# Kernel tuning notes

Hardware: AMD Instinct MI355X
Metric: run time of the kernel (lower is better)

The kernel has to match this reference:

```python
import jax, jax.numpy as jnp
import numpy as np

LN_EPS = 1e-5

def _proj(x, w, b):
    # 1x1 conv: x [B,C,H,W], w [O,C], b [O]
    return jnp.einsum('bchw,oc->bohw', x, w) + b[None, :, None, None]

def _layernorm(x, w, b):
    # normalize over last dim
    mu = jnp.mean(x, axis=-1, keepdims=True)
    var = jnp.mean(jnp.square(x - mu), axis=-1, keepdims=True)
    return (x - mu) * jax.lax.rsqrt(var + LN_EPS) * w + b

def setup_inputs() -> dict:
    key = jax.random.key(0)
    ks = jax.random.split(key, 12)
    C = 256
    d = {
        's3': jax.random.normal(ks[0], (2, C, 64, 64), jnp.float32),
        's4': jax.random.normal(ks[1], (2, C, 32, 64), jnp.float32),
        's5': jax.random.normal(ks[2], (2, C, 16, 64), jnp.float32),
        'qw': jax.random.normal(ks[3], (C, C), jnp.float32) * 0.02,
        'qb': jax.random.normal(ks[4], (C,), jnp.float32) * 0.02,
        'kw': jax.random.normal(ks[5], (C, C), jnp.float32) * 0.02,
        'kb': jax.random.normal(ks[6], (C,), jnp.float32) * 0.02,
        'vw': jax.random.normal(ks[7], (C, C), jnp.float32) * 0.02,
        'vb': jax.random.normal(ks[8], (C,), jnp.float32) * 0.02,
        'ow': jax.random.normal(ks[9], (C, C), jnp.float32) * 0.02,
        'ob': jax.random.normal(ks[10], (C,), jnp.float32) * 0.02,
        'ln_w': jnp.ones((C,), jnp.float32),
        'ln_b': jnp.zeros((C,), jnp.float32),
    }
    return d

def reference(s3, s4, s5, qw, qb, kw, kb, vw, vb, ow, ob, ln_w, ln_b):
    B, C, H, W = s3.shape
    num_heads = 8
    head_dim = C // num_heads
    scale = head_dim ** -0.5

    q = _proj(s3, qw, qb).reshape(B, C, H * W)            # [B,C,Nq]
    k4 = _proj(s4, kw, kb).reshape(B, C, -1)
    k5 = _proj(s5, kw, kb).reshape(B, C, -1)
    v4 = _proj(s4, vw, vb).reshape(B, C, -1)
    v5 = _proj(s5, vw, vb).reshape(B, C, -1)
    k = jnp.concatenate([k4, k5], axis=-1)                # [B,C,Nk]
    v = jnp.concatenate([v4, v5], axis=-1)

    # [B,C,N] -> [B,h,N,d]
    def split_heads(t):
        Bn, Cn, N = t.shape
        return t.transpose(0, 2, 1).reshape(Bn, N, num_heads, head_dim).transpose(0, 2, 1, 3)

    qh, kh, vh = split_heads(q), split_heads(k), split_heads(v)
    attn = jnp.einsum('bhqd,bhkd->bhqk', qh, kh) * scale
    attn = jax.nn.softmax(attn, axis=-1)
    out = jnp.einsum('bhqk,bhkd->bhqd', attn, vh)         # [B,h,Nq,d]
    out = out.transpose(0, 2, 1, 3).reshape(B, H * W, C)  # [B,Nq,C]
    out = out.transpose(0, 2, 1).reshape(B, C, H, W)
    out = _proj(out, ow, ob)
    out = s3 + out
    out_flat = out.reshape(B, C, H * W).transpose(0, 2, 1)  # [B,N,C]
    out_flat = _layernorm(out_flat, ln_w, ln_b)
    return out_flat.transpose(0, 2, 1).reshape(B, C, H, W)
```

## Files before the change

### kernel.cpp

```cpp
#include <hip/hip_runtime.h>

typedef __bf16 bf16;
typedef __bf16 bf16x4 __attribute__((ext_vector_type(4)));
typedef __bf16 bf16x8 __attribute__((ext_vector_type(8)));
typedef _Float16 f16;
typedef _Float16 f16x2 __attribute__((ext_vector_type(2)));
typedef _Float16 f16x8 __attribute__((ext_vector_type(8)));
typedef float f32x4 __attribute__((ext_vector_type(4)));
typedef unsigned int u32x4 __attribute__((ext_vector_type(4)));

#define MFMA16 __builtin_amdgcn_mfma_f32_16x16x32_bf16
#define MFMA16H __builtin_amdgcn_mfma_f32_16x16x32_f16

__device__ __forceinline__ void async16(void* lds, const void* g) {
    __builtin_amdgcn_global_load_lds((const __attribute__((address_space(1))) unsigned int*)g,
                                     (__attribute__((address_space(3))) unsigned int*)lds, 16, 0, 0);
}

__device__ __forceinline__ f16x2 pkrtz(float a, float b) {
    return __builtin_bit_cast(f16x2, __builtin_amdgcn_cvt_pkrtz(a, b));
}

__device__ __forceinline__ float fdot2h(f16x2 a, f16x2 b, float c) {
#if __has_builtin(__builtin_amdgcn_fdot2)
    return __builtin_amdgcn_fdot2(a, b, c, false);
#else
    return c + (float)a[0] * (float)b[0] + (float)a[1] * (float)b[1];
#endif
}

__global__ __launch_bounds__(256) void k_prep(const float* __restrict__ qw, const float* __restrict__ kw,
                                              const float* __restrict__ vw, const float* __restrict__ ow,
                                              bf16* __restrict__ Wb,
                                              const float* __restrict__ s3, const float* __restrict__ s4,
                                              const float* __restrict__ s5,
                                              bf16* __restrict__ s3t, bf16* __restrict__ s45t) {
    __shared__ float T[64][65];
    int bx = blockIdx.x, t = threadIdx.x;
    if (bx < 256) {
        int tt = bx * 256 + t;
        const float* srcs[4] = {qw, kw, vw, ow};
        int which = tt >> 14;
        int idx = (tt & 16383) * 4;
        f32x4 v = *(const f32x4*)(srcs[which] + idx);
        bf16x4 o;
        o[0] = (bf16)v[0]; o[1] = (bf16)v[1]; o[2] = (bf16)v[2]; o[3] = (bf16)v[3];
        *(bf16x4*)(Wb + (size_t)which * 65536 + idx) = o;
        return;
    }
    const float* src; bf16* dst; int N, dstRows, rowOff, x, y, z;
    if (bx < 768)       { int i = bx - 256;  src = s3; dst = s3t;  N = 4096; dstRows = 4096; rowOff = 0;    x = i & 63; y = (i >> 6) & 3; z = i >> 8; }
    else if (bx < 1024) { int i = bx - 768;  src = s4; dst = s45t; N = 2048; dstRows = 3072; rowOff = 0;    x = i & 31; y = (i >> 5) & 3; z = i >> 7; }
    else                { int i = bx - 1024; src = s5; dst = s45t; N = 1024; dstRows = 3072; rowOff = 2048; x = i & 15; y = (i >> 4) & 3; z = i >> 6; }
    int c0 = y * 64, n0 = x * 64, b = z;
    const float* s = src + ((size_t)b * 256 + c0) * N + n0;
#pragma unroll
    for (int i = 0; i < 4; i++) {
        int flat = i * 256 + t;
        int row = flat >> 4;
        int col = (flat & 15) * 4;
        f32x4 v = *(const f32x4*)(s + (size_t)row * N + col);
        T[row][col + 0] = v[0]; T[row][col + 1] = v[1];
        T[row][col + 2] = v[2]; T[row][col + 3] = v[3];
    }
    __syncthreads();
#pragma unroll
    for (int i = 0; i < 4; i++) {
        int flat = i * 256 + t;
        int nrow = flat >> 4;
        int c4 = (flat & 15) * 4;
        bf16x4 o;
        o[0] = (bf16)T[c4 + 0][nrow]; o[1] = (bf16)T[c4 + 1][nrow];
        o[2] = (bf16)T[c4 + 2][nrow]; o[3] = (bf16)T[c4 + 3][nrow];
        *(bf16x4*)(dst + ((size_t)(b * dstRows + rowOff + n0 + nrow)) * 256 + c0 + c4) = o;
    }
}

__global__ __launch_bounds__(256) void k_qkv(const bf16* __restrict__ Wb,
                                             const bf16* __restrict__ s3t, const bf16* __restrict__ s45t,
                                             const float* __restrict__ qb, const float* __restrict__ kb,
                                             const float* __restrict__ vb,
                                             bf16* __restrict__ Qb, bf16* __restrict__ Kb,
                                             f16* __restrict__ Vtb, float qscale) {
    int i = blockIdx.x;
    int mode, n0, m0, b, Nrows;
    const bf16 *A, *Bt; const float* bias; float oscale = 1.0f;
    if (i < 512) {
        mode = 0; A = Wb; Bt = s3t; bias = qb; Nrows = 4096; oscale = qscale;
        n0 = (i & 63) * 64; m0 = ((i >> 6) & 3) * 64; b = i >> 8;
    } else if (i < 896) {
        unsigned j = i - 512;
        mode = 1; A = Wb + 65536; Bt = s45t; bias = kb; Nrows = 3072;
        n0 = (j % 48u) * 64; unsigned rr = j / 48u; m0 = (rr & 3) * 64; b = rr >> 2;
    } else {
        unsigned j = i - 896;
        mode = 2; A = Wb + 131072; Bt = s45t; bias = vb; Nrows = 3072;
        n0 = (j % 48u) * 64; unsigned rr = j / 48u; m0 = (rr & 3) * 64; b = rr >> 2;
    }
    __shared__ bf16 As[64 * 40];
    __shared__ bf16 Bs[64 * 40];
    int t = threadIdx.x;
    int w = t >> 6, lane = t & 63;
    int lrow = lane & 15, lk = lane >> 4;
    f32x4 acc[4] = {};
    int r = t >> 2, cc = (t & 3) * 8;
    for (int kc = 0; kc < 256; kc += 32) {
        u32x4 va = *(const u32x4*)(A + (size_t)(m0 + r) * 256 + kc + cc);
        u32x4 vbv = *(const u32x4*)(Bt + ((size_t)b * Nrows + n0 + r) * 256 + kc + cc);
        *(u32x4*)(As + r * 40 + cc) = va;
        *(u32x4*)(Bs + r * 40 + cc) = vbv;
        __syncthreads();
        bf16x8 af = *(const bf16x8*)(As + (w * 16 + lrow) * 40 + lk * 8);
#pragma unroll
        for (int ct = 0; ct < 4; ct++) {
            bf16x8 bfr = *(const bf16x8*)(Bs + (ct * 16 + lrow) * 40 + lk * 8);
            acc[ct] = MFMA16(af, bfr, acc[ct], 0, 0, 0);
        }
        __syncthreads();
    }
    int o0 = m0 + w * 16 + lk * 4;
    f32x4 b4 = *(const f32x4*)(bias + o0);
    int head = o0 >> 5;
#pragma unroll
    for (int ct = 0; ct < 4; ct++) {
        int n = n0 + ct * 16 + lrow;
        if (mode == 0) {
            int dd = o0 & 31;
            bf16x4 pv;
#pragma unroll
            for (int j = 0; j < 4; j++) pv[j] = (bf16)((acc[ct][j] + b4[j]) * oscale);
            *(bf16x4*)(Qb + ((size_t)(b * 8 + head) * 4096 + n) * 32 + dd) = pv;
        } else if (mode == 1) {
            int dd = o0 & 31;
            int u = n & 31;
            int np = (n & ~31) | (((u >> 2) & 1) << 4) | ((u >> 3) << 2) | (u & 3);
            bf16x4 pv;
#pragma unroll
            for (int j = 0; j < 4; j++) pv[j] = (bf16)(acc[ct][j] + b4[j]);
            *(bf16x4*)(Kb + ((size_t)(b * 8 + head) * 3072 + np) * 32 + dd) = pv;
        } else {
            int g = (n & 63) >> 3;
#pragma unroll
            for (int j = 0; j < 4; j++) {
                int dd = (o0 & 31) + j;
                int col = (n & ~63) + ((g ^ (dd & 7)) << 3) + (n & 7);
                Vtb[((size_t)(b * 8 + head) * 32 + dd) * 3072 + col] = (f16)(acc[ct][j] + b4[j]);
            }
        }
    }
}

__global__ __launch_bounds__(256, 4) void k_attn(const bf16* __restrict__ Q, const bf16* __restrict__ K,
                                                 const f16* __restrict__ Vt,
                                                 f16* __restrict__ Opart, float* __restrict__ Lsum) {
    int bh = blockIdx.y;
    int q0 = blockIdx.x * 256;
    int sp = blockIdx.z;
    int kn0 = sp * 768;
    int t = threadIdx.x, w = t >> 6, lane = t & 63;
    int lrow = lane & 15, lk = lane >> 4;
    __shared__ bf16 Ks[2][64 * 32];
    __shared__ f16 Vs[2][32 * 64];
    __shared__ f16 Tq[4][32 * 66];
    const bf16* kbase = K + (size_t)bh * 3072 * 32;
    const f16* vbase = Vt + (size_t)bh * 32 * 3072;
    const bf16* kg = kbase + (size_t)(kn0 + w * 16 + (lane >> 2)) * 32 + (lane & 3) * 8;
    const f16* vg = vbase + (size_t)(w * 8 + (lane >> 3)) * 3072 + kn0 + (lane & 7) * 8;
    bf16x8 aq[4];
#pragma unroll
    for (int qg = 0; qg < 4; ++qg)
        aq[qg] = *(const bf16x8*)(Q + ((size_t)bh * 4096 + q0 + w * 64 + qg * 16 + lrow) * 32 + lk * 8);
    f32x4 accO[4][2] = {};
    float lsum[4] = {0.f, 0.f, 0.f, 0.f};
    f32x4 zero = {};
    f16x2 one2; one2[0] = (f16)1.f; one2[1] = (f16)1.f;
    int vkey = lrow & 7;
    async16(&Ks[0][w * 512], kg);
    async16(&Vs[0][w * 512], vg);
    __syncthreads();
    for (int c = 0; c < 12; ++c) {
        int buf = c & 1;
        if (c < 11) {
            async16(&Ks[buf ^ 1][w * 512], kg + (size_t)(c + 1) * 64 * 32);
            async16(&Vs[buf ^ 1][w * 512], vg + (c + 1) * 64);
        }
        const bf16* ksb = &Ks[buf][0];
        const f16* vsb = &Vs[buf][0];
#pragma unroll
        for (int p = 0; p < 2; ++p) {
            f32x4 s[2][4];
#pragma unroll
            for (int t2 = 0; t2 < 2; ++t2) {
                bf16x8 kf = *(const bf16x8*)(ksb + (p * 32 + t2 * 16 + lrow) * 32 + lk * 8);
#pragma unroll
                for (int qg = 0; qg < 4; ++qg) s[t2][qg] = MFMA16(kf, aq[qg], zero, 0, 0, 0);
            }
            f16x8 p8[4];
#pragma unroll
            for (int qg = 0; qg < 4; ++qg) {
                f16x2 h0 = pkrtz(__builtin_amdgcn_exp2f(s[0][qg][0]), __builtin_amdgcn_exp2f(s[0][qg][1]));
                f16x2 h1 = pkrtz(__builtin_amdgcn_exp2f(s[0][qg][2]), __builtin_amdgcn_exp2f(s[0][qg][3]));
                f16x2 h2 = pkrtz(__builtin_amdgcn_exp2f(s[1][qg][0]), __builtin_amdgcn_exp2f(s[1][qg][1]));
                f16x2 h3 = pkrtz(__builtin_amdgcn_exp2f(s[1][qg][2]), __builtin_amdgcn_exp2f(s[1][qg][3]));
                f16x8 pk;
                pk[0] = h0[0]; pk[1] = h0[1]; pk[2] = h1[0]; pk[3] = h1[1];
                pk[4] = h2[0]; pk[5] = h2[1]; pk[6] = h3[0]; pk[7] = h3[1];
                p8[qg] = pk;
                lsum[qg] = fdot2h(h0, one2, lsum[qg]);
                lsum[qg] = fdot2h(h1, one2, lsum[qg]);
                lsum[qg] = fdot2h(h2, one2, lsum[qg]);
                lsum[qg] = fdot2h(h3, one2, lsum[qg]);
            }
#pragma unroll
            for (int dh = 0; dh < 2; ++dh) {
                f16x8 vf = *(const f16x8*)(vsb + (dh * 16 + lrow) * 64 + ((((p << 2) | lk) ^ vkey) << 3));
#pragma unroll
                for (int qg = 0; qg < 4; ++qg)
                    accO[qg][dh] = MFMA16H(vf, p8[qg], accO[qg][dh], 0, 0, 0);
            }
        }
        __syncthreads();
    }
    int sb = sp * 16 + bh;
#pragma unroll
    for (int qg = 0; qg < 4; ++qg) {
        lsum[qg] += __shfl_xor(lsum[qg], 16, 64);
        lsum[qg] += __shfl_xor(lsum[qg], 32, 64);
    }
    if (lane < 16) {
#pragma unroll
        for (int qg = 0; qg < 4; ++qg)
            Lsum[(size_t)sb * 4096 + q0 + w * 64 + qg * 16 + lane] = lsum[qg];
    }
    f16* tw = &Tq[w][0];
#pragma unroll
    for (int qg = 0; qg < 4; ++qg)
#pragma unroll
        for (int dh = 0; dh < 2; ++dh)
#pragma unroll
            for (int i = 0; i < 4; ++i)
                tw[(dh * 16 + lk * 4 + i) * 66 + qg * 16 + lrow] = (f16)accO[qg][dh][i];
    int q4 = (lane & 15) * 4, dgrp = (lane >> 4) * 8;
#pragma unroll
    for (int qq = 0; qq < 4; ++qq) {
        f16x8 ov;
#pragma unroll
        for (int dj = 0; dj < 8; ++dj) ov[dj] = tw[(dgrp + dj) * 66 + q4 + qq];
        *(f16x8*)(Opart + ((size_t)sb * 4096 + q0 + w * 64 + q4 + qq) * 32 + dgrp) = ov;
    }
}

__global__ __launch_bounds__(256) void k_oproj(const bf16* __restrict__ A, const f16* __restrict__ Opart,
                                               const float* __restrict__ Ls, const float* __restrict__ bias,
                                               float* __restrict__ opre) {
    int i = blockIdx.x;
    int n0 = (i & 63) * 64, m0 = ((i >> 6) & 3) * 64, b = i >> 8;
    __shared__ bf16 As[64 * 40];
    __shared__ bf16 Bs[64 * 40];
    int t = threadIdx.x;
    int w = t >> 6, lane = t & 63;
    int lrow = lane & 15, lk = lane >> 4;
    f32x4 acc[4] = {};
    int r = t >> 2, cc = (t & 3) * 8;
    int q = n0 + r;
    const size_t SPS = (size_t)16 * 4096 * 32;
    for (int kc = 0; kc < 256; kc += 32) {
        int bh = b * 8 + (kc >> 5);
        u32x4 va = *(const u32x4*)(A + (size_t)(m0 + r) * 256 + kc + cc);
        float l = Ls[(size_t)bh * 4096 + q] + Ls[(size_t)(16 + bh) * 4096 + q] +
                  Ls[(size_t)(32 + bh) * 4096 + q] + Ls[(size_t)(48 + bh) * 4096 + q];
        float rl = 1.0f / l;
        const f16* ob = Opart + ((size_t)bh * 4096 + q) * 32 + cc;
        f16x8 a0 = *(const f16x8*)(ob);
        f16x8 a1 = *(const f16x8*)(ob + SPS);
        f16x8 a2 = *(const f16x8*)(ob + 2 * SPS);
        f16x8 a3 = *(const f16x8*)(ob + 3 * SPS);
        bf16x8 bb;
#pragma unroll
        for (int j = 0; j < 8; ++j)
            bb[j] = (bf16)((((float)a0[j] + (float)a1[j]) + ((float)a2[j] + (float)a3[j])) * rl);
        *(u32x4*)(As + r * 40 + cc) = va;
        *(bf16x8*)(Bs + r * 40 + cc) = bb;
        __syncthreads();
        bf16x8 af = *(const bf16x8*)(As + (w * 16 + lrow) * 40 + lk * 8);
#pragma unroll
        for (int ct = 0; ct < 4; ct++) {
            bf16x8 bfr = *(const bf16x8*)(Bs + (ct * 16 + lrow) * 40 + lk * 8);
            acc[ct] = MFMA16(af, bfr, acc[ct], 0, 0, 0);
        }
        __syncthreads();
    }
    int o0 = m0 + w * 16 + lk * 4;
    f32x4 b4 = *(const f32x4*)(bias + o0);
#pragma unroll
    for (int ct = 0; ct < 4; ct++) {
        int n = n0 + ct * 16 + lrow;
        f32x4 v;
#pragma unroll
        for (int j = 0; j < 4; j++) v[j] = acc[ct][j] + b4[j];
        *(f32x4*)(opre + ((size_t)b * 4096 + n) * 256 + o0) = v;
    }
}

__global__ __launch_bounds__(256) void k_ln(const float* __restrict__ opre, const float* __restrict__ s3,
                                            const float* __restrict__ lnw, const float* __restrict__ lnb,
                                            float* __restrict__ out) {
    int b = blockIdx.y;
    int n0 = blockIdx.x * 32;
    __shared__ float T[32][257];
    __shared__ float mu_s[32], rs_s[32];
    int t = threadIdx.x;
#pragma unroll
    for (int i = 0; i < 8; i++) {
        int flat = i * 256 + t;
        int n = flat >> 6;
        int c = (flat & 63) * 4;
        f32x4 v = *(const f32x4*)(opre + ((size_t)b * 4096 + n0 + n) * 256 + c);
        T[n][c + 0] = v[0]; T[n][c + 1] = v[1]; T[n][c + 2] = v[2]; T[n][c + 3] = v[3];
    }
    __syncthreads();
#pragma unroll
    for (int i = 0; i < 8; i++) {
        int flat = i * 256 + t;
        int c = flat >> 3;
        int n = (flat & 7) * 4;
        f32x4 v = *(const f32x4*)(s3 + ((size_t)b * 256 + c) * 4096 + n0 + n);
        T[n + 0][c] += v[0]; T[n + 1][c] += v[1]; T[n + 2][c] += v[2]; T[n + 3][c] += v[3];
    }
    __syncthreads();
    int w = t >> 6, lane = t & 63;
    for (int j = 0; j < 8; j++) {
        int row = w * 8 + j;
        float x0 = T[row][lane], x1 = T[row][lane + 64];
        float x2 = T[row][lane + 128], x3 = T[row][lane + 192];
        float s = x0 + x1 + x2 + x3;
        float s2 = x0 * x0 + x1 * x1 + x2 * x2 + x3 * x3;
#pragma unroll
        for (int off = 1; off < 64; off <<= 1) {
            s += __shfl_xor(s, off, 64);
            s2 += __shfl_xor(s2, off, 64);
        }
        if (lane == 0) {
            float mu = s * (1.0f / 256.0f);
            float var = s2 * (1.0f / 256.0f) - mu * mu;
            mu_s[row] = mu;
            rs_s[row] = rsqrtf(var + 1e-5f);
        }
    }
    __syncthreads();
    int c = t;
    float wv = lnw[c], bv = lnb[c];
#pragma unroll
    for (int i = 0; i < 8; i++) {
        int n = i * 4;
        f32x4 o;
#pragma unroll
        for (int k = 0; k < 4; k++)
            o[k] = (T[n + k][c] - mu_s[n + k]) * rs_s[n + k] * wv + bv;
        *(f32x4*)(out + ((size_t)b * 256 + c) * 4096 + n0 + n) = o;
    }
}

extern "C" void kernel_launch(void* const* d_in, const int* in_sizes, int n_in,
                              void* d_out, int out_size, void* d_ws, size_t ws_size,
                              hipStream_t stream) {
    const float* s3  = (const float*)d_in[0];
    const float* s4  = (const float*)d_in[1];
    const float* s5  = (const float*)d_in[2];
    const float* qw  = (const float*)d_in[3];
    const float* qb  = (const float*)d_in[4];
    const float* kw  = (const float*)d_in[5];
    const float* kb  = (const float*)d_in[6];
    const float* vw  = (const float*)d_in[7];
    const float* vb  = (const float*)d_in[8];
    const float* ow  = (const float*)d_in[9];
    const float* ob  = (const float*)d_in[10];
    const float* lnw = (const float*)d_in[11];
    const float* lnb = (const float*)d_in[12];
    float* out = (float*)d_out;
    char* ws = (char*)d_ws;

    bf16* Wb    = (bf16*)(ws);
    bf16* s3t   = (bf16*)(ws + (512ull << 10));
    bf16* s45t  = (bf16*)(ws + (4608ull << 10));
    bf16* Qb    = (bf16*)(ws + (7680ull << 10));
    bf16* Kb    = Qb + (2ull * 8 * 4096 * 32);
    f16*  Vtb   = (f16*)(Kb + (2ull * 8 * 3072 * 32));
    f16*  Opart = (f16*)(ws + (17920ull << 10));
    float* Lsum = (float*)(ws + (34304ull << 10));
    float* opre = (float*)(ws + (512ull << 10));

    const float qscale = 0.17677669529663688f * 1.4426950408889634f;

    k_prep<<<1152, 256, 0, stream>>>(qw, kw, vw, ow, Wb, s3, s4, s5, s3t, s45t);
    k_qkv<<<1280, 256, 0, stream>>>(Wb, s3t, s45t, qb, kb, vb, Qb, Kb, Vtb, qscale);
    k_attn<<<dim3(16, 16, 4), 256, 0, stream>>>(Qb, Kb, Vtb, Opart, Lsum);
    k_oproj<<<512, 256, 0, stream>>>(Wb + 196608, Opart, Lsum, ob, opre);
    k_ln<<<dim3(128, 2), 256, 0, stream>>>(opre, s3, lnw, lnb, out);
}
```

Baseline: 154.7 us.

## Fuse output projection with residual layernorm and split attention keys six ways

Merges the output projection and the residual+layernorm kernels into one kernel. Each block computes all 256 output channels for 32 queries, adds the bf16 residual from the transposed s3 copy, and normalizes in shared memory, so the fp32 intermediate no longer round-trips through global memory. The attention split-K grows from 4 to 6 partitions. Shared memory is aliased and the launch bound raised to 6 blocks to improve occupancy. This costs more partial-output traffic and a bf16 residual instead of fp32, which loses some precision.

```diff
diff --git a/kernel.cpp b/kernel.cpp
--- a/kernel.cpp
+++ b/kernel.cpp
@@ -5,6 +5,7 @@
 typedef __bf16 bf16x8 __attribute__((ext_vector_type(8)));
 typedef _Float16 f16;
 typedef _Float16 f16x2 __attribute__((ext_vector_type(2)));
+typedef _Float16 f16x4 __attribute__((ext_vector_type(4)));
 typedef _Float16 f16x8 __attribute__((ext_vector_type(8)));
 typedef float f32x4 __attribute__((ext_vector_type(4)));
 typedef unsigned int u32x4 __attribute__((ext_vector_type(4)));
@@ -150,18 +151,19 @@
     }
 }
 
-__global__ __launch_bounds__(256, 4) void k_attn(const bf16* __restrict__ Q, const bf16* __restrict__ K,
+__global__ __launch_bounds__(256, 6) void k_attn(const bf16* __restrict__ Q, const bf16* __restrict__ K,
                                                  const f16* __restrict__ Vt,
                                                  f16* __restrict__ Opart, float* __restrict__ Lsum) {
     int bh = blockIdx.y;
     int q0 = blockIdx.x * 256;
     int sp = blockIdx.z;
-    int kn0 = sp * 768;
+    int kn0 = sp * 512;
     int t = threadIdx.x, w = t >> 6, lane = t & 63;
     int lrow = lane & 15, lk = lane >> 4;
-    __shared__ bf16 Ks[2][64 * 32];
-    __shared__ f16 Vs[2][32 * 64];
-    __shared__ f16 Tq[4][32 * 66];
+    __shared__ __align__(16) char smem[16896];
+    bf16* Ks = (bf16*)smem;
+    f16* Vs = (f16*)(smem + 8192);
+    f16* Tq = (f16*)smem;
     const bf16* kbase = K + (size_t)bh * 3072 * 32;
     const f16* vbase = Vt + (size_t)bh * 32 * 3072;
     const bf16* kg = kbase + (size_t)(kn0 + w * 16 + (lane >> 2)) * 32 + (lane & 3) * 8;
@@ -175,17 +177,17 @@
     f32x4 zero = {};
     f16x2 one2; one2[0] = (f16)1.f; one2[1] = (f16)1.f;
     int vkey = lrow & 7;
-    async16(&Ks[0][w * 512], kg);
-    async16(&Vs[0][w * 512], vg);
+    async16(Ks + w * 512, kg);
+    async16(Vs + w * 512, vg);
     __syncthreads();
-    for (int c = 0; c < 12; ++c) {
+    for (int c = 0; c < 8; ++c) {
         int buf = c & 1;
-        if (c < 11) {
-            async16(&Ks[buf ^ 1][w * 512], kg + (size_t)(c + 1) * 64 * 32);
-            async16(&Vs[buf ^ 1][w * 512], vg + (c + 1) * 64);
-        }
-        const bf16* ksb = &Ks[buf][0];
-        const f16* vsb = &Vs[buf][0];
+        if (c < 7) {
+            async16(Ks + (buf ^ 1) * 2048 + w * 512, kg + (size_t)(c + 1) * 64 * 32);
+            async16(Vs + (buf ^ 1) * 2048 + w * 512, vg + (c + 1) * 64);
+        }
+        const bf16* ksb = Ks + buf * 2048;
+        const f16* vsb = Vs + buf * 2048;
 #pragma unroll
         for (int p = 0; p < 2; ++p) {
             f32x4 s[2][4];
@@ -232,7 +234,7 @@
         for (int qg = 0; qg < 4; ++qg)
             Lsum[(size_t)sb * 4096 + q0 + w * 64 + qg * 16 + lane] = lsum[qg];
     }
-    f16* tw = &Tq[w][0];
+    f16* tw = Tq + w * 2112;
 #pragma unroll
     for (int qg = 0; qg < 4; ++qg)
 #pragma unroll
@@ -250,114 +252,117 @@
     }
 }
 
-__global__ __launch_bounds__(256) void k_oproj(const bf16* __restrict__ A, const f16* __restrict__ Opart,
-                                               const float* __restrict__ Ls, const float* __restrict__ bias,
-                                               float* __restrict__ opre) {
+__global__ __launch_bounds__(256) void k_oln(const bf16* __restrict__ A, const f16* __restrict__ Opart,
+                                             const float* __restrict__ Ls, const float* __restrict__ bias,
+                                             const bf16* __restrict__ s3t,
+                                             const float* __restrict__ lnw, const float* __restrict__ lnb,
+                                             float* __restrict__ out) {
     int i = blockIdx.x;
-    int n0 = (i & 63) * 64, m0 = ((i >> 6) & 3) * 64, b = i >> 8;
-    __shared__ bf16 As[64 * 40];
-    __shared__ bf16 Bs[64 * 40];
-    int t = threadIdx.x;
-    int w = t >> 6, lane = t & 63;
+    int b = i >> 7, n0 = (i & 127) * 32;
+    __shared__ __align__(16) char smem[34176];
+    bf16* As = (bf16*)smem;
+    bf16* Bs = (bf16*)(smem + 20480);
+    float* T = (float*)smem;
+    float* ps = (float*)(smem + 32896);
+    float* pq = (float*)(smem + 33408);
+    float* mu_s = (float*)(smem + 33920);
+    float* rs_s = (float*)(smem + 34048);
+    int t = threadIdx.x, w = t >> 6, lane = t & 63;
     int lrow = lane & 15, lk = lane >> 4;
-    f32x4 acc[4] = {};
-    int r = t >> 2, cc = (t & 3) * 8;
-    int q = n0 + r;
+    f32x4 acc[4][2] = {};
+    int rB = t >> 3, cgB = (t & 7) * 4;
+    int q = n0 + rB;
     const size_t SPS = (size_t)16 * 4096 * 32;
     for (int kc = 0; kc < 256; kc += 32) {
         int bh = b * 8 + (kc >> 5);
-        u32x4 va = *(const u32x4*)(A + (size_t)(m0 + r) * 256 + kc + cc);
-        float l = Ls[(size_t)bh * 4096 + q] + Ls[(size_t)(16 + bh) * 4096 + q] +
-                  Ls[(size_t)(32 + bh) * 4096 + q] + Ls[(size_t)(48 + bh) * 4096 + q];
+        const bf16* ar = A + (size_t)t * 256 + kc;
+        u32x4 va0 = *(const u32x4*)(ar);
+        u32x4 va1 = *(const u32x4*)(ar + 8);
+        u32x4 va2 = *(const u32x4*)(ar + 16);
+        u32x4 va3 = *(const u32x4*)(ar + 24);
+        float l = 0.f;
+#pragma unroll
+        for (int sp = 0; sp < 6; ++sp) l += Ls[(size_t)(sp * 16 + bh) * 4096 + q];
         float rl = 1.0f / l;
-        const f16* ob = Opart + ((size_t)bh * 4096 + q) * 32 + cc;
-        f16x8 a0 = *(const f16x8*)(ob);
-        f16x8 a1 = *(const f16x8*)(ob + SPS);
-        f16x8 a2 = *(const f16x8*)(ob + 2 * SPS);
-        f16x8 a3 = *(const f16x8*)(ob + 3 * SPS);
-        bf16x8 bb;
-#pragma unroll
-        for (int j = 0; j < 8; ++j)
-            bb[j] = (bf16)((((float)a0[j] + (float)a1[j]) + ((float)a2[j] + (float)a3[j])) * rl);
-        *(u32x4*)(As + r * 40 + cc) = va;
-        *(bf16x8*)(Bs + r * 40 + cc) = bb;
+        const f16* obp = Opart + ((size_t)bh * 4096 + q) * 32 + cgB;
+        f32x4 sv = {};
+#pragma unroll
+        for (int sp = 0; sp < 6; ++sp) {
+            f16x4 av = *(const f16x4*)(obp + sp * SPS);
+#pragma unroll
+            for (int j = 0; j < 4; ++j) sv[j] += (float)av[j];
+        }
+        bf16x4 bb;
+#pragma unroll
+        for (int j = 0; j < 4; ++j) bb[j] = (bf16)(sv[j] * rl);
+        *(u32x4*)(As + t * 40 + 0) = va0;
+        *(u32x4*)(As + t * 40 + 8) = va1;
+        *(u32x4*)(As + t * 40 + 16) = va2;
+        *(u32x4*)(As + t * 40 + 24) = va3;
+        *(bf16x4*)(Bs + rB * 40 + cgB) = bb;
         __syncthreads();
-        bf16x8 af = *(const bf16x8*)(As + (w * 16 + lrow) * 40 + lk * 8);
-#pragma unroll
-        for (int ct = 0; ct < 4; ct++) {
-            bf16x8 bfr = *(const bf16x8*)(Bs + (ct * 16 + lrow) * 40 + lk * 8);
-            acc[ct] = MFMA16(af, bfr, acc[ct], 0, 0, 0);
+#pragma unroll
+        for (int mt = 0; mt < 4; ++mt) {
+            bf16x8 af = *(const bf16x8*)(As + (mt * 64 + w * 16 + lrow) * 40 + lk * 8);
+#pragma unroll
+            for (int ct = 0; ct < 2; ++ct) {
+                bf16x8 bfr = *(const bf16x8*)(Bs + (ct * 16 + lrow) * 40 + lk * 8);
+                acc[mt][ct] = MFMA16(af, bfr, acc[mt][ct], 0, 0, 0);
+            }
         }
         __syncthreads();
     }
-    int o0 = m0 + w * 16 + lk * 4;
-    f32x4 b4 = *(const f32x4*)(bias + o0);
-#pragma unroll
-    for (int ct = 0; ct < 4; ct++) {
-        int n = n0 + ct * 16 + lrow;
-        f32x4 v;
-#pragma unroll
-        for (int j = 0; j < 4; j++) v[j] = acc[ct][j] + b4[j];
-        *(f32x4*)(opre + ((size_t)b * 4096 + n) * 256 + o0) = v;
-    }
-}
-
-__global__ __launch_bounds__(256) void k_ln(const float* __restrict__ opre, const float* __restrict__ s3,
-                                            const float* __restrict__ lnw, const float* __restrict__ lnb,
-                                            float* __restrict__ out) {
-    int b = blockIdx.y;
-    int n0 = blockIdx.x * 32;
-    __shared__ float T[32][257];
-    __shared__ float mu_s[32], rs_s[32];
-    int t = threadIdx.x;
-#pragma unroll
-    for (int i = 0; i < 8; i++) {
-        int flat = i * 256 + t;
-        int n = flat >> 6;
-        int c = (flat & 63) * 4;
-        f32x4 v = *(const f32x4*)(opre + ((size_t)b * 4096 + n0 + n) * 256 + c);
-        T[n][c + 0] = v[0]; T[n][c + 1] = v[1]; T[n][c + 2] = v[2]; T[n][c + 3] = v[3];
+    float wsum[2] = {0.f, 0.f}, wsq[2] = {0.f, 0.f};
+#pragma unroll
+    for (int ct = 0; ct < 2; ++ct) {
+        int n = ct * 16 + lrow;
+#pragma unroll
+        for (int mt = 0; mt < 4; ++mt) {
+            int c0 = mt * 64 + w * 16 + lk * 4;
+            f32x4 b4 = *(const f32x4*)(bias + c0);
+            bf16x4 rv = *(const bf16x4*)(s3t + ((size_t)b * 4096 + n0 + n) * 256 + c0);
+#pragma unroll
+            for (int j = 0; j < 4; ++j) {
+                float v = acc[mt][ct][j] + b4[j] + (float)rv[j];
+                T[n * 257 + c0 + j] = v;
+                wsum[ct] += v;
+                wsq[ct] += v * v;
+            }
+        }
+    }
+#pragma unroll
+    for (int ct = 0; ct < 2; ++ct) {
+        wsum[ct] += __shfl_xor(wsum[ct], 16, 64);
+        wsum[ct] += __shfl_xor(wsum[ct], 32, 64);
+        wsq[ct] += __shfl_xor(wsq[ct], 16, 64);
+        wsq[ct] += __shfl_xor(wsq[ct], 32, 64);
+    }
+    if (lk == 0) {
+#pragma unroll
+        for (int ct = 0; ct < 2; ++ct) {
+            ps[w * 32 + ct * 16 + lrow] = wsum[ct];
+            pq[w * 32 + ct * 16 + lrow] = wsq[ct];
+        }
     }
     __syncthreads();
-#pragma unroll
-    for (int i = 0; i < 8; i++) {
-        int flat = i * 256 + t;
-        int c = flat >> 3;
-        int n = (flat & 7) * 4;
-        f32x4 v = *(const f32x4*)(s3 + ((size_t)b * 256 + c) * 4096 + n0 + n);
-        T[n + 0][c] += v[0]; T[n + 1][c] += v[1]; T[n + 2][c] += v[2]; T[n + 3][c] += v[3];
+    if (t < 32) {
+        float S = ps[t] + ps[32 + t] + ps[64 + t] + ps[96 + t];
+        float Q2 = pq[t] + pq[32 + t] + pq[64 + t] + pq[96 + t];
+        float m = S * (1.0f / 256.0f);
+        mu_s[t] = m;
+        rs_s[t] = rsqrtf(Q2 * (1.0f / 256.0f) - m * m + 1e-5f);
     }
     __syncthreads();
-    int w = t >> 6, lane = t & 63;
-    for (int j = 0; j < 8; j++) {
-        int row = w * 8 + j;
-        float x0 = T[row][lane], x1 = T[row][lane + 64];
-        float x2 = T[row][lane + 128], x3 = T[row][lane + 192];
-        float s = x0 + x1 + x2 + x3;
-        float s2 = x0 * x0 + x1 * x1 + x2 * x2 + x3 * x3;
-#pragma unroll
-        for (int off = 1; off < 64; off <<= 1) {
-            s += __shfl_xor(s, off, 64);
-            s2 += __shfl_xor(s2, off, 64);
-        }
-        if (lane == 0) {
-            float mu = s * (1.0f / 256.0f);
-            float var = s2 * (1.0f / 256.0f) - mu * mu;
-            mu_s[row] = mu;
-            rs_s[row] = rsqrtf(var + 1e-5f);
-        }
-    }
-    __syncthreads();
-    int c = t;
-    float wv = lnw[c], bv = lnb[c];
-#pragma unroll
-    for (int i = 0; i < 8; i++) {
-        int n = i * 4;
+    int cb = t >> 3, n4 = (t & 7) * 4;
+#pragma unroll
+    for (int cc8 = 0; cc8 < 8; ++cc8) {
+        int c = cb + cc8 * 32;
+        float wv = lnw[c], bv = lnb[c];
         f32x4 o;
 #pragma unroll
-        for (int k = 0; k < 4; k++)
-            o[k] = (T[n + k][c] - mu_s[n + k]) * rs_s[n + k] * wv + bv;
-        *(f32x4*)(out + ((size_t)b * 256 + c) * 4096 + n0 + n) = o;
+        for (int k2 = 0; k2 < 4; ++k2)
+            o[k2] = (T[(n4 + k2) * 257 + c] - mu_s[n4 + k2]) * rs_s[n4 + k2] * wv + bv;
+        *(f32x4*)(out + ((size_t)b * 256 + c) * 4096 + n0 + n4) = o;
     }
 }
 
@@ -387,14 +392,12 @@
     bf16* Kb    = Qb + (2ull * 8 * 4096 * 32);
     f16*  Vtb   = (f16*)(Kb + (2ull * 8 * 3072 * 32));
     f16*  Opart = (f16*)(ws + (17920ull << 10));
-    float* Lsum = (float*)(ws + (34304ull << 10));
-    float* opre = (float*)(ws + (512ull << 10));
+    float* Lsum = (float*)(ws + (42496ull << 10));
 
     const float qscale = 0.17677669529663688f * 1.4426950408889634f;
 
     k_prep<<<1152, 256, 0, stream>>>(qw, kw, vw, ow, Wb, s3, s4, s5, s3t, s45t);
     k_qkv<<<1280, 256, 0, stream>>>(Wb, s3t, s45t, qb, kb, vb, Qb, Kb, Vtb, qscale);
-    k_attn<<<dim3(16, 16, 4), 256, 0, stream>>>(Qb, Kb, Vtb, Opart, Lsum);
-    k_oproj<<<512, 256, 0, stream>>>(Wb + 196608, Opart, Lsum, ob, opre);
-    k_ln<<<dim3(128, 2), 256, 0, stream>>>(opre, s3, lnw, lnb, out);
-}
+    k_attn<<<dim3(16, 16, 6), 256, 0, stream>>>(Qb, Kb, Vtb, Opart, Lsum);
+    k_oln<<<256, 256, 0, stream>>>(Wb + 196608, Opart, Lsum, ob, s3t, lnw, lnb, out);
+}
```

Result: slower. 248.0 us (+60.3%).
